# Performance work log

Hardware: AMD Instinct MI355X
Metric: run time of the kernel (lower is better)

Reference implementation:

```python
import jax, jax.numpy as jnp
import numpy as np
from jax import lax

FI, FO, K, EPS = 512, 256, 3, 1e-06


def _fir_kernel(gain):
    f = jnp.array([1.0, 3.0, 3.0, 1.0], dtype=jnp.float32)
    f = f[None, :] * f[:, None]
    f = f / f.sum() * gain  # (4,4), symmetric so conv-vs-correlation flip is a no-op
    return f


def setup_inputs() -> dict:
    key = jax.random.key(0)
    k1, k2 = jax.random.split(key)
    x = jax.random.normal(k1, (8, FI, 64, 64), dtype=jnp.float32)
    w = jax.random.normal(k2, (1, FO, FI, K, K), dtype=jnp.float32)
    return {"x": x, "w": w}


def reference(x, w):
    w_scale = (FI * K * K) ** (-0.5)
    wm = w[0] * w_scale  # (fo, fi, k, k); per-sample scale is constant across batch
    demod = lax.rsqrt(jnp.sum(wm * wm, axis=(1, 2, 3)) + EPS)  # (fo,)
    wm = wm * demod[:, None, None, None]
    # torch conv_transpose2d(stride=2, padding=0) with weight (fi, fo, k, k) where
    # weight[i, o] = wm[o, i]  ==  dilated conv with kernel flip(wm) OIHW, pad k-1=2.
    kern = wm[:, :, ::-1, ::-1]
    y = lax.conv_general_dilated(
        x, kern, window_strides=(1, 1), padding=[(2, 2), (2, 2)],
        lhs_dilation=(2, 2), dimension_numbers=("NCHW", "OIHW", "NCHW"))
    # upFirDn2D with scale=2, conv_k=3: p=0 -> pad (1,1) both dims, filter gain 4
    f = _fir_kernel(4.0)
    C = y.shape[1]
    fk = jnp.broadcast_to(f[None, None], (C, 1, 4, 4))
    y = lax.conv_general_dilated(
        y, fk, window_strides=(1, 1), padding=[(1, 1), (1, 1)],
        feature_group_count=C, dimension_numbers=("NCHW", "OIHW", "NCHW"))
    return y  # (8, 256, 128, 128)
```

## Files before the change

### kernel.cpp

```cpp
#include <hip/hip_runtime.h>

typedef unsigned short u16;
typedef unsigned int u32;
typedef __attribute__((ext_vector_type(8))) short bf16x8;
typedef __attribute__((ext_vector_type(4))) float f32x4;

#define XP_BYTES 35684352
#define YB_BYTES 68714544
#define HY_OFF   (XP_BYTES + YB_BYTES)
#define WS_NEED  ((size_t)HY_OFF + 2359296)
#define CS 16776

__device__ inline u16 f2bf(float f) {
  union { float f; unsigned u; } v; v.f = f;
  unsigned r = v.u + 0x7fffu + ((v.u >> 16) & 1u);
  return (u16)(r >> 16);
}

__device__ inline void gl_lds16(const u16* g, u16* l) {
  __builtin_amdgcn_global_load_lds(
      (const __attribute__((address_space(1))) unsigned int*)g,
      (__attribute__((address_space(3))) unsigned int*)l, 16, 0, 0);
}

__global__ void xprep(const float* __restrict__ x, u16* __restrict__ xp) {
  __shared__ float tile[64 * 65];
  int bid = blockIdx.x;
  int cc = bid & 7, h = (bid >> 3) & 63, n = bid >> 9;
  int c0 = cc * 64;
  int t = threadIdx.x;
  const float* xb = x + ((size_t)(n * 512 + c0) * 64 + h) * 64;
  for (int r = 0; r < 16; ++r) {
    int flat = r * 256 + t;
    int ci = flat >> 6, w = flat & 63;
    tile[w * 65 + ci] = xb[(size_t)ci * 4096 + w];
  }
  __syncthreads();
  u16* xpb = xp + ((size_t)(n * 66 + h + 1) * 66 + 1) * 512 + c0;
  for (int r = 0; r < 8; ++r) {
    int flat = r * 256 + t;
    int pr = flat & 31;
    int w = flat >> 5;
    int ci = pr * 2;
    float v0 = tile[w * 65 + ci], v1 = tile[w * 65 + ci + 1];
    unsigned pk = (unsigned)f2bf(v0) | ((unsigned)f2bf(v1) << 16);
    *(unsigned*)(xpb + (size_t)w * 512 + ci) = pk;
  }
  u16* rowbase = xp + ((size_t)(n * 66 + h + 1) * 66) * 512 + c0;
  if (t < 32) *(u32*)(rowbase + 2 * t) = 0u;
  else if (t < 64) *(u32*)(rowbase + (size_t)65 * 512 + 2 * (t - 32)) = 0u;
  if (h == 0) {
    u16* r0 = xp + ((size_t)(n * 66) * 66) * 512 + c0;
    for (int j = t; j < 2112; j += 256) {
      int col = j >> 5, wi = j & 31;
      *(u32*)(r0 + (size_t)col * 512 + 2 * wi) = 0u;
    }
  }
  if (h == 63) {
    u16* r65 = xp + ((size_t)(n * 66 + 65) * 66) * 512 + c0;
    for (int j = t; j < 2112; j += 256) {
      int col = j >> 5, wi = j & 31;
      *(u32*)(r65 + (size_t)col * 512 + 2 * wi) = 0u;
    }
  }
}

__global__ void wprep9(const float* __restrict__ w, u16* __restrict__ Hy) {
  __shared__ float wl[4608];
  __shared__ float red[256];
  int o = blockIdx.x, t = threadIdx.x;
  const float* wo = w + (size_t)o * 4608;
  float s = 0.f;
  for (int j = t; j < 4608; j += 256) { float v = wo[j]; wl[j] = v; s += v * v; }
  red[t] = s;
  __syncthreads();
  for (int st = 128; st; st >>= 1) { if (t < st) red[t] += red[t + st]; __syncthreads(); }
  float demod = rsqrtf(red[0] * (1.0f / 4608.0f) + 1e-6f);
  float scale = demod * 0.014731391274719739f;
  const int DY[9] = {0, 2, 0, 2, 0, 2, 1, 1, 1};
  const int DX[9] = {0, 0, 2, 2, 1, 1, 0, 2, 1};
  for (int i = t; i < 512; i += 256) {
#pragma unroll
    for (int pl = 0; pl < 9; ++pl) {
      float g = wl[i * 9 + DY[pl] * 3 + DX[pl]] * scale;
      Hy[(size_t)pl * 131072 + (size_t)o * 512 + i] = f2bf(g);
    }
  }
}

#define BARR() __builtin_amdgcn_s_barrier()
#define WAITL() do { asm volatile("s_waitcnt lgkmcnt(0)" ::: "memory"); __builtin_amdgcn_sched_barrier(0); } while (0)
#define WAITV4() do { asm volatile("s_waitcnt vmcnt(4)" ::: "memory"); __builtin_amdgcn_sched_barrier(0); } while (0)
#define WAITV0() do { asm volatile("s_waitcnt vmcnt(0)" ::: "memory"); __builtin_amdgcn_sched_barrier(0); } while (0)

__device__ __forceinline__ void rdA8(const u16* sb, int rbase, int grp, bf16x8 af[4][2]) {
#pragma unroll
  for (int ti = 0; ti < 4; ++ti) {
    int r = rbase + ti * 16;
    int x7 = r & 7;
#pragma unroll
    for (int ks = 0; ks < 2; ++ks) {
      int ch = (ks * 4 + grp) ^ x7;
      af[ti][ks] = *(const bf16x8*)(sb + r * 64 + ch * 8);
    }
  }
}

__device__ __forceinline__ void rdB4(const u16* sb, int rbase, int grp, bf16x8 bfr[2][2]) {
#pragma unroll
  for (int tj = 0; tj < 2; ++tj) {
    int r = rbase + tj * 16;
    int x7 = r & 7;
#pragma unroll
    for (int ks = 0; ks < 2; ++ks) {
      int ch = (ks * 4 + grp) ^ x7;
      bfr[tj][ks] = *(const bf16x8*)(sb + 16384 + r * 64 + ch * 8);
    }
  }
}

template <int MI, int NI>
__device__ __forceinline__ void qmfma(const bf16x8 af[4][2], const bf16x8 bfr[2][2],
                                      f32x4 acc[8][4]) {
#pragma unroll
  for (int ti = 0; ti < 4; ++ti)
#pragma unroll
    for (int tj = 0; tj < 2; ++tj)
#pragma unroll
      for (int ks = 0; ks < 2; ++ks)
        acc[MI * 4 + ti][NI * 2 + tj] = __builtin_amdgcn_mfma_f32_16x16x32_bf16(
            af[ti][ks], bfr[tj][ks], acc[MI * 4 + ti][NI * 2 + tj], 0, 0, 0);
}

__device__ __forceinline__ void stA2(const u16* __restrict__ xp, u16* d0, u16* d1,
                                     int tile, int NK, u32 a0, u32 a1,
                                     u32 adj1, u32 adj2, u32 adj3) {
  if (tile < NK) {
    int tap = tile >> 3;
    u32 ko = (u32)((tile & 7) << 6);
    u32 adj = tap == 0 ? 0u : (tap == 1 ? adj1 : (tap == 2 ? adj2 : adj3));
    gl_lds16(xp + (a0 - adj + ko), d0);
    gl_lds16(xp + (a1 - adj + ko), d1);
  }
}

__device__ __forceinline__ void stB2(const u16* __restrict__ hb, u16* d0, u16* d1,
                                     int tile, int NK, u32 b0, u32 b1) {
  if (tile < NK) {
    int tap = tile >> 3;
    u32 ko = (u32)((tile & 7) << 6);
    const u16* hp = hb + (size_t)tap * 131072;
    gl_lds16(hp + (b0 + ko), d0);
    gl_lds16(hp + (b1 + ko), d1);
  }
}

__global__ __launch_bounds__(512, 2) void conv_y(const u16* __restrict__ xp,
                                                 const u16* __restrict__ Hy,
                                                 u16* __restrict__ yb) {
  __shared__ __align__(16) u16 su[65536];

  int bid = blockIdx.x;
  int t = threadIdx.x;
  int wid = t >> 6, lane = t & 63;

  int img = bid & 7;
  int kk = bid >> 3;
  int mt, Wp, CNT, NTAP, PB, PO, STLIM;
  u32 adj1 = 0, adj2 = 0, adj3 = 0;
  if (kk < 17)      { mt = kk;      Wp = 66; CNT = 4290; NTAP = 4; PB = 0; PO = 0;     STLIM = 4296;
                      adj1 = 33792u; adj2 = 512u; adj3 = 34304u; }
  else if (kk < 34) { mt = kk - 17; Wp = 64; CNT = 4160; NTAP = 2; PB = 4; PO = 4296;  STLIM = 4160;
                      adj1 = 33792u; }
  else if (kk < 51) { mt = kk - 34; Wp = 66; CNT = 4224; NTAP = 2; PB = 6; PO = 8456;  STLIM = 4224;
                      adj1 = 512u; }
  else              { mt = kk - 51; Wp = 64; CNT = 4096; NTAP = 1; PB = 8; PO = 12680; STLIM = 4096; }

  int m0 = mt * 256;
  int NK = NTAP * 8;
  int NITER = NTAP * 4;
  const u16* hb = Hy + (size_t)PB * 131072;

  int wm = wid >> 2, wn = wid & 3;
  int la = lane & 15, grp = lane >> 4;

  int rho = t >> 3;
  int gch = (t & 7) ^ (rho & 7);

  u32 gA[4], gB[4];
#pragma unroll
  for (int i = 0; i < 4; ++i) {
    int m = m0 + i * 64 + rho;
    if (m > CNT - 1) m = CNT - 1;
    u32 a = (u32)m / (u32)Wp;
    u32 b = (u32)m - a * (u32)Wp;
    gA[i] = (u32)(((img * 66 + a + 1) * 66 + (b + 1)) * 512 + gch * 8);
    gB[i] = (u32)((i * 64 + rho) * 512 + gch * 8);
  }
  u16* sw = su + wid * 512;

  f32x4 acc[8][4];
#pragma unroll
  for (int i = 0; i < 8; ++i)
#pragma unroll
    for (int j = 0; j < 4; ++j) acc[i][j] = (f32x4){0.f, 0.f, 0.f, 0.f};

  stB2(hb, sw + 16384, sw + 20480, 0, NK, gB[0], gB[1]);
  stB2(hb, sw + 24576, sw + 28672, 0, NK, gB[2], gB[3]);
  stA2(xp, sw, sw + 4096, 0, NK, gA[0], gA[1], adj1, adj2, adj3);
  stA2(xp, sw + 8192, sw + 12288, 0, NK, gA[2], gA[3], adj1, adj2, adj3);
  stB2(hb, sw + 49152, sw + 53248, 1, NK, gB[0], gB[1]);
  stB2(hb, sw + 57344, sw + 61440, 1, NK, gB[2], gB[3]);
  WAITV4();
  BARR();

  bf16x8 af[4][2], bf0[2][2], bf1[2][2];

#pragma unroll 1
  for (int it = 0; it < NITER; ++it) {
    int t0 = 2 * it;
    bool more = (it + 1 < NITER);

    rdA8(su, wm * 128 + la, grp, af);
    rdB4(su, wn * 64 + la, grp, bf0);
    stA2(xp, sw + 32768, sw + 36864, t0 + 1, NK, gA[0], gA[1], adj1, adj2, adj3);
    BARR(); WAITL();
    __builtin_amdgcn_s_setprio(1); qmfma<0, 0>(af, bf0, acc); __builtin_amdgcn_s_setprio(0);
    BARR();
    rdB4(su, wn * 64 + 32 + la, grp, bf1);
    stA2(xp, sw + 40960, sw + 45056, t0 + 1, NK, gA[2], gA[3], adj1, adj2, adj3);
    BARR(); WAITL();
    __builtin_amdgcn_s_setprio(1); qmfma<0, 1>(af, bf1, acc); __builtin_amdgcn_s_setprio(0);
    BARR();
    rdA8(su, wm * 128 + 64 + la, grp, af);
    stB2(hb, sw + 16384, sw + 20480, t0 + 2, NK, gB[0], gB[1]);
    BARR(); WAITL();
    __builtin_amdgcn_s_setprio(1); qmfma<1, 1>(af, bf1, acc); __builtin_amdgcn_s_setprio(0);
    BARR();
    stB2(hb, sw + 24576, sw + 28672, t0 + 2, NK, gB[2], gB[3]);
    BARR(); WAITL();
    __builtin_amdgcn_s_setprio(1); qmfma<1, 0>(af, bf0, acc); __builtin_amdgcn_s_setprio(0);
    if (more) { WAITV4(); } else { WAITV0(); }
    BARR();
    rdA8(su + 32768, wm * 128 + la, grp, af);
    rdB4(su + 32768, wn * 64 + la, grp, bf0);
    stA2(xp, sw, sw + 4096, t0 + 2, NK, gA[0], gA[1], adj1, adj2, adj3);
    BARR(); WAITL();
    __builtin_amdgcn_s_setprio(1); qmfma<0, 0>(af, bf0, acc); __builtin_amdgcn_s_setprio(0);
    BARR();
    rdB4(su + 32768, wn * 64 + 32 + la, grp, bf1);
    stA2(xp, sw + 8192, sw + 12288, t0 + 2, NK, gA[2], gA[3], adj1, adj2, adj3);
    BARR(); WAITL();
    __builtin_amdgcn_s_setprio(1); qmfma<0, 1>(af, bf1, acc); __builtin_amdgcn_s_setprio(0);
    BARR();
    rdA8(su + 32768, wm * 128 + 64 + la, grp, af);
    stB2(hb, sw + 49152, sw + 53248, t0 + 3, NK, gB[0], gB[1]);
    BARR(); WAITL();
    __builtin_amdgcn_s_setprio(1); qmfma<1, 1>(af, bf1, acc); __builtin_amdgcn_s_setprio(0);
    BARR();
    stB2(hb, sw + 57344, sw + 61440, t0 + 3, NK, gB[2], gB[3]);
    BARR(); WAITL();
    __builtin_amdgcn_s_setprio(1); qmfma<1, 0>(af, bf0, acc); __builtin_amdgcn_s_setprio(0);
    if (more) { WAITV4(); }
    BARR();
  }

  WAITV0();
  __syncthreads();
#pragma unroll
  for (int nj = 0; nj < 4; ++nj) {
    int orow = wn * 64 + nj * 16 + la;
    int x7 = orow & 7;
#pragma unroll
    for (int mi8 = 0; mi8 < 8; ++mi8)
#pragma unroll
      for (int jp = 0; jp < 2; ++jp) {
        int ml = wm * 128 + mi8 * 16 + grp * 4 + jp * 2;
        u32 pk = (u32)f2bf(acc[mi8][nj][jp * 2]) |
                 ((u32)f2bf(acc[mi8][nj][jp * 2 + 1]) << 16);
        *(u32*)(su + orow * 256 + (((ml >> 3) ^ x7) * 8) + (ml & 7)) = pk;
      }
  }
  __syncthreads();
  {
    u16* ybp = yb + 8;
    int o = t >> 1, s = t & 1;
    size_t gb = (size_t)(img * 256 + o) * CS + PO + m0 + s * 128;
    int x7 = o & 7;
#pragma unroll
    for (int i = 0; i < 16; ++i) {
      int mo = s * 128 + i * 8;
      if (m0 + mo < STLIM)
        *(bf16x8*)(ybp + gb + i * 8) = *(const bf16x8*)(su + o * 256 + (((mo >> 3) ^ x7) * 8));
    }
  }
}

__global__ void fir2(const u16* __restrict__ yb, float* __restrict__ z) {
  int flat = blockIdx.x * 256 + threadIdx.x;
  int qh = flat & 15, phb = (flat >> 4) & 31, o = (flat >> 9) & 255, n = flat >> 17;
  const u16* cb = yb + 8 + (size_t)(n * 256 + o) * CS;
  int a0 = 2 * phb - 1;
  int b0 = 4 * qh - 1;

  float out[4][8];
#pragma unroll
  for (int i = 0; i < 4; ++i)
#pragma unroll
    for (int j = 0; j < 8; ++j) out[i][j] = 0.f;

  const int PO_[4] = {0, 4296, 8456, 12680};
  const int WP_[4] = {66, 64, 66, 64};
  const int HA_[4] = {65, 65, 64, 64};
  const int WB_[4] = {65, 64, 65, 64};

#pragma unroll
  for (int ph = 0; ph < 4; ++ph) {
    int rp = ph >> 1, rq = ph & 1;
    const u16* pb = cb + PO_[ph];
    float hcol[4][8];
#pragma unroll
    for (int la = 0; la < 4; ++la) {
      if (rp == 0 && la == 0) continue;
      int ag = a0 + la;
      bool rv = (ag >= 0) && (ag < HA_[ph]);
      const u16* rb = pb + (ag * WP_[ph] + b0 - 1);
      u32 ls[4];
      ls[0] = *(const u32*)(rb);
      ls[1] = *(const u32*)(rb + 2);
      ls[2] = *(const u32*)(rb + 4);
      ls[3] = *(const u32*)(rb + 6);
      float v[6];
#pragma unroll
      for (int lb = 0; lb < 6; ++lb) {
        int jj = lb + 1;
        u32 w16 = (jj & 1) ? (ls[jj >> 1] >> 16) : (ls[jj >> 1] & 0xffffu);
        float fv = __uint_as_float(w16 << 16);
        int bg = b0 + lb;
        bool ok = rv && (bg >= 0) && (bg < WB_[ph]);
        v[lb] = ok ? fv : 0.f;
      }
#pragma unroll
      for (int e = 0; e < 4; ++e) {
        if (rq == 0) {
          hcol[la][2 * e]     = 3.f * v[e + 1] + v[e + 2];
          hcol[la][2 * e + 1] = v[e + 1] + 3.f * v[e + 2];
        } else {
          hcol[la][2 * e]     = v[e] + 3.f * v[e + 1];
          hcol[la][2 * e + 1] = 3.f * v[e + 1] + v[e + 2];
        }
      }
    }
#pragma unroll
    for (int jq = 0; jq < 8; ++jq) {
      if (rp == 0) {
        out[0][jq] += 3.f * hcol[1][jq] + hcol[2][jq];
        out[1][jq] += hcol[1][jq] + 3.f * hcol[2][jq];
        out[2][jq] += 3.f * hcol[2][jq] + hcol[3][jq];
        out[3][jq] += hcol[2][jq] + 3.f * hcol[3][jq];
      } else {
        out[0][jq] += hcol[0][jq] + 3.f * hcol[1][jq];
        out[1][jq] += 3.f * hcol[1][jq] + hcol[2][jq];
        out[2][jq] += hcol[1][jq] + 3.f * hcol[2][jq];
        out[3][jq] += 3.f * hcol[2][jq] + hcol[3][jq];
      }
    }
  }

  float* zb = z + ((size_t)(n * 256 + o) * 128 + phb * 4) * 128 + qh * 8;
#pragma unroll
  for (int ip = 0; ip < 4; ++ip) {
    f32x4 v0, v1;
#pragma unroll
    for (int j = 0; j < 4; ++j) { v0[j] = out[ip][j] * 0.0625f; v1[j] = out[ip][j + 4] * 0.0625f; }
    *(f32x4*)(zb + (size_t)ip * 128) = v0;
    *(f32x4*)(zb + (size_t)ip * 128 + 4) = v1;
  }
}

__global__ void wprep36(const float* __restrict__ w, u16* __restrict__ Hm) {
  __shared__ float wl[4608];
  __shared__ float red[256];
  int o = blockIdx.x, t = threadIdx.x;
  const float* wo = w + (size_t)o * 4608;
  float s = 0.f;
  for (int j = t; j < 4608; j += 256) { float v = wo[j]; wl[j] = v; s += v * v; }
  red[t] = s;
  __syncthreads();
  for (int st = 128; st; st >>= 1) { if (t < st) red[t] += red[t + st]; __syncthreads(); }
  float demod = rsqrtf(red[0] * (1.0f / 4608.0f) + 1e-6f);
  float scale = demod * 0.014731391274719739f;
  const float F1[4] = {1.f, 3.f, 3.f, 1.f};
  for (int i = t; i < 512; i += 256) {
    float wm[9];
    for (int k = 0; k < 9; ++k) wm[k] = wl[i * 9 + k] * scale;
    for (int rp = 0; rp < 2; ++rp)
      for (int rq = 0; rq < 2; ++rq)
        for (int u = 0; u < 3; ++u)
          for (int v = 0; v < 3; ++v) {
            int s_ = 2 - 2 * u + rp, t_ = 2 - 2 * v + rq;
            float g = 0.f;
            for (int dy = 0; dy < 3; ++dy) {
              int a = dy + 1 - s_;
              if (a < 0 || a > 3) continue;
              for (int dx = 0; dx < 3; ++dx) {
                int b = dx + 1 - t_;
                if (b < 0 || b > 3) continue;
                g += wm[dy * 3 + dx] * (F1[a] * F1[b]);
              }
            }
            g *= 0.0625f;
            Hm[(size_t)((rp * 2 + rq) * 9 + u * 3 + v) * 131072 + (size_t)o * 512 + i] = f2bf(g);
          }
  }
}

__global__ __launch_bounds__(256) void conv_main(const u16* __restrict__ xp,
                                                 const u16* __restrict__ Hm,
                                                 float* __restrict__ z) {
  __shared__ __align__(16) float smemf[8448];
  u16* su = (u16*)smemf;
  int bid = blockIdx.x;
  int sub = bid & 7;
  int rp = sub >> 2;
  int o0 = (sub & 3) * 64;
  int mtile = bid >> 3;
  int n_img = mtile >> 5;
  int hp0 = (mtile & 31) * 2;
  int t = threadIdx.x;
  int wave = t >> 6, lane = t & 63;
  int wm0 = (wave & 1) * 64;
  int wn0 = (wave >> 1) * 32;
  int la = lane & 15;
  int ks = (lane >> 4) * 8;
  int rsel = t >> 2;
  int koff = (t & 3) * 8;
  f32x4 acc[2][4][2];
#pragma unroll
  for (int a = 0; a < 2; ++a)
#pragma unroll
    for (int b = 0; b < 4; ++b)
#pragma unroll
      for (int c = 0; c < 2; ++c)
        acc[a][b][c] = (f32x4){0.f, 0.f, 0.f, 0.f};
#pragma unroll 1
  for (int tap = 0; tap < 9; ++tap) {
    int du = tap / 3, dv = tap - du * 3;
    const u16* gA0 = xp + ((size_t)(n_img * 66 + hp0 + du) * 66 + dv) * 512;
    const u16* gB0 = Hm + (size_t)(rp * 18 + tap) * 131072 + (size_t)(o0 + rsel) * 512 + koff;
    const u16* gAr0 = gA0 + (size_t)rsel * 512 + koff;
    const u16* gAr1 = gA0 + (size_t)(66 + rsel) * 512 + koff;
#pragma unroll 1
    for (int kc = 0; kc < 16; ++kc) {
      int c0 = kc * 32;
      __syncthreads();
      gl_lds16(gAr0 + c0, su + wave * 512);
      gl_lds16(gAr1 + c0, su + 2048 + wave * 512);
      gl_lds16(gB0 + c0,              su + 4096 + wave * 512);
      gl_lds16(gB0 + 9 * 131072 + c0, su + 6144 + wave * 512);
      __syncthreads();
      bf16x8 af[4];
#pragma unroll
      for (int ti = 0; ti < 4; ++ti)
        af[ti] = *(const bf16x8*)(su + (wm0 + ti * 16 + la) * 32 + ks);
      bf16x8 bfr[2][2];
#pragma unroll
      for (int rqq = 0; rqq < 2; ++rqq)
#pragma unroll
        for (int tj = 0; tj < 2; ++tj)
          bfr[rqq][tj] = *(const bf16x8*)(su + 4096 + rqq * 2048 + (wn0 + tj * 16 + la) * 32 + ks);
#pragma unroll
      for (int rqq = 0; rqq < 2; ++rqq)
#pragma unroll
        for (int ti = 0; ti < 4; ++ti)
#pragma unroll
          for (int tj = 0; tj < 2; ++tj)
            acc[rqq][ti][tj] = __builtin_amdgcn_mfma_f32_16x16x32_bf16(
                af[ti], bfr[rqq][tj], acc[rqq][ti][tj], 0, 0, 0);
    }
  }
  __syncthreads();
  float* lws = smemf + wave * 2112;
  int p = 2 * (hp0 + (wave & 1)) + rp;
#pragma unroll
  for (int tj = 0; tj < 2; ++tj) {
#pragma unroll
    for (int rqq = 0; rqq < 2; ++rqq)
#pragma unroll
      for (int ti = 0; ti < 4; ++ti) {
        int wqb = ti * 16 + (lane >> 4) * 4;
        f32x4 v = acc[rqq][ti][tj];
#pragma unroll
        for (int r = 0; r < 4; ++r)
          lws[la * 132 + 2 * (wqb + r) + rqq] = v[r];
      }
    __syncthreads();
    int obase = o0 + wn0 + tj * 16;
#pragma unroll
    for (int c = 0; c < 8; ++c) {
      int idx = c * 64 + lane;
      int ol = idx >> 5, q4 = (idx & 31) * 4;
      f32x4 vv = *(const f32x4*)(lws + ol * 132 + q4);
      *(f32x4*)(z + (((size_t)n_img * 256 + obase + ol) * 128 + p) * 128 + q4) = vv;
    }
    __syncthreads();
  }
}

extern "C" void kernel_launch(void* const* d_in, const int* in_sizes, int n_in,
                              void* d_out, int out_size, void* d_ws, size_t ws_size,
                              hipStream_t stream) {
  const float* x = (const float*)d_in[0];
  const float* w = (const float*)d_in[1];
  float* z = (float*)d_out;
  u16* xp = (u16*)d_ws;

  if (ws_size >= WS_NEED) {
    u16* yb = (u16*)((char*)d_ws + XP_BYTES);
    u16* hy = (u16*)((char*)d_ws + HY_OFF);
    xprep<<<4096, 256, 0, stream>>>(x, xp);
    wprep9<<<256, 256, 0, stream>>>(w, hy);
    conv_y<<<536, 512, 0, stream>>>(xp, hy, yb);
    fir2<<<4096, 256, 0, stream>>>(yb, z);
  } else {
    u16* Hm = (u16*)((char*)d_ws + XP_BYTES);
    hipMemsetAsync(xp, 0, XP_BYTES, stream);
    xprep<<<4096, 256, 0, stream>>>(x, xp);
    wprep36<<<256, 256, 0, stream>>>(w, Hm);
    conv_main<<<2048, 256, 0, stream>>>(xp, Hm, z);
  }
}
```

Measured before the change: 315.0 us.

## Halve conv GEMM N-tile and K-step to fit more blocks per CU

The conv_y GEMM tile shrinks from 256x256 to 256x128 output channels and the K step from 64 to 32. Shared memory drops from 128KB to 48KB and launch bounds rise to 4 blocks per SM, doubling the grid to 1072 blocks. The aim is higher occupancy and better CU fill, with more blocks to hide memory latency. The cost is halved reuse of A tiles, twice as many pipeline iterations with barriers, and an epilogue split into two passes.

```diff
diff --git a/kernel.cpp b/kernel.cpp
--- a/kernel.cpp
+++ b/kernel.cpp
@@ -90,75 +90,56 @@
 
 #define BARR() __builtin_amdgcn_s_barrier()
 #define WAITL() do { asm volatile("s_waitcnt lgkmcnt(0)" ::: "memory"); __builtin_amdgcn_sched_barrier(0); } while (0)
-#define WAITV4() do { asm volatile("s_waitcnt vmcnt(4)" ::: "memory"); __builtin_amdgcn_sched_barrier(0); } while (0)
+#define WAITV1() do { asm volatile("s_waitcnt vmcnt(1)" ::: "memory"); __builtin_amdgcn_sched_barrier(0); } while (0)
 #define WAITV0() do { asm volatile("s_waitcnt vmcnt(0)" ::: "memory"); __builtin_amdgcn_sched_barrier(0); } while (0)
 
-__device__ __forceinline__ void rdA8(const u16* sb, int rbase, int grp, bf16x8 af[4][2]) {
+__device__ __forceinline__ void rdA4(const u16* sb, int rbase, int grp, bf16x8 af[4]) {
 #pragma unroll
   for (int ti = 0; ti < 4; ++ti) {
     int r = rbase + ti * 16;
-    int x7 = r & 7;
-#pragma unroll
-    for (int ks = 0; ks < 2; ++ks) {
-      int ch = (ks * 4 + grp) ^ x7;
-      af[ti][ks] = *(const bf16x8*)(sb + r * 64 + ch * 8);
-    }
-  }
-}
-
-__device__ __forceinline__ void rdB4(const u16* sb, int rbase, int grp, bf16x8 bfr[2][2]) {
-#pragma unroll
-  for (int tj = 0; tj < 2; ++tj) {
-    int r = rbase + tj * 16;
-    int x7 = r & 7;
-#pragma unroll
-    for (int ks = 0; ks < 2; ++ks) {
-      int ch = (ks * 4 + grp) ^ x7;
-      bfr[tj][ks] = *(const bf16x8*)(sb + 16384 + r * 64 + ch * 8);
-    }
-  }
+    int ch = grp ^ (r & 3);
+    af[ti] = *(const bf16x8*)(sb + r * 32 + ch * 8);
+  }
+}
+
+__device__ __forceinline__ bf16x8 rdB1(const u16* sb, int r, int grp) {
+  int ch = grp ^ (r & 3);
+  return *(const bf16x8*)(sb + 8192 + r * 32 + ch * 8);
 }
 
 template <int MI, int NI>
-__device__ __forceinline__ void qmfma(const bf16x8 af[4][2], const bf16x8 bfr[2][2],
-                                      f32x4 acc[8][4]) {
+__device__ __forceinline__ void qmfma4(const bf16x8 af[4], bf16x8 bf,
+                                       f32x4 acc[8][2]) {
 #pragma unroll
   for (int ti = 0; ti < 4; ++ti)
-#pragma unroll
-    for (int tj = 0; tj < 2; ++tj)
-#pragma unroll
-      for (int ks = 0; ks < 2; ++ks)
-        acc[MI * 4 + ti][NI * 2 + tj] = __builtin_amdgcn_mfma_f32_16x16x32_bf16(
-            af[ti][ks], bfr[tj][ks], acc[MI * 4 + ti][NI * 2 + tj], 0, 0, 0);
-}
-
-__device__ __forceinline__ void stA2(const u16* __restrict__ xp, u16* d0, u16* d1,
-                                     int tile, int NK, u32 a0, u32 a1,
+    acc[MI * 4 + ti][NI] = __builtin_amdgcn_mfma_f32_16x16x32_bf16(
+        af[ti], bf, acc[MI * 4 + ti][NI], 0, 0, 0);
+}
+
+__device__ __forceinline__ void stA1(const u16* __restrict__ xp, u16* d,
+                                     int tile, int NK, u32 a,
                                      u32 adj1, u32 adj2, u32 adj3) {
   if (tile < NK) {
-    int tap = tile >> 3;
-    u32 ko = (u32)((tile & 7) << 6);
+    int tap = tile >> 4;
+    u32 ko = (u32)((tile & 15) << 5);
     u32 adj = tap == 0 ? 0u : (tap == 1 ? adj1 : (tap == 2 ? adj2 : adj3));
-    gl_lds16(xp + (a0 - adj + ko), d0);
-    gl_lds16(xp + (a1 - adj + ko), d1);
-  }
-}
-
-__device__ __forceinline__ void stB2(const u16* __restrict__ hb, u16* d0, u16* d1,
-                                     int tile, int NK, u32 b0, u32 b1) {
+    gl_lds16(xp + (a - adj + ko), d);
+  }
+}
+
+__device__ __forceinline__ void stB1(const u16* __restrict__ hb, u16* d,
+                                     int tile, int NK, u32 b) {
   if (tile < NK) {
-    int tap = tile >> 3;
-    u32 ko = (u32)((tile & 7) << 6);
-    const u16* hp = hb + (size_t)tap * 131072;
-    gl_lds16(hp + (b0 + ko), d0);
-    gl_lds16(hp + (b1 + ko), d1);
-  }
-}
-
-__global__ __launch_bounds__(512, 2) void conv_y(const u16* __restrict__ xp,
+    int tap = tile >> 4;
+    u32 ko = (u32)((tile & 15) << 5);
+    gl_lds16(hb + (size_t)tap * 131072 + (b + ko), d);
+  }
+}
+
+__global__ __launch_bounds__(512, 4) void conv_y(const u16* __restrict__ xp,
                                                  const u16* __restrict__ Hy,
                                                  u16* __restrict__ yb) {
-  __shared__ __align__(16) u16 su[65536];
+  __shared__ __align__(16) u16 su[24576];
 
   int bid = blockIdx.x;
   int t = threadIdx.x;
@@ -166,133 +147,141 @@
 
   int img = bid & 7;
   int kk = bid >> 3;
-  int mt, Wp, CNT, NTAP, PB, PO, STLIM;
+  int mt, oh, Wp, CNT, NTAP, PB, PO, STLIM;
   u32 adj1 = 0, adj2 = 0, adj3 = 0;
-  if (kk < 17)      { mt = kk;      Wp = 66; CNT = 4290; NTAP = 4; PB = 0; PO = 0;     STLIM = 4296;
-                      adj1 = 33792u; adj2 = 512u; adj3 = 34304u; }
-  else if (kk < 34) { mt = kk - 17; Wp = 64; CNT = 4160; NTAP = 2; PB = 4; PO = 4296;  STLIM = 4160;
-                      adj1 = 33792u; }
-  else if (kk < 51) { mt = kk - 34; Wp = 66; CNT = 4224; NTAP = 2; PB = 6; PO = 8456;  STLIM = 4224;
-                      adj1 = 512u; }
-  else              { mt = kk - 51; Wp = 64; CNT = 4096; NTAP = 1; PB = 8; PO = 12680; STLIM = 4096; }
+  if (kk < 34)       { int k2 = kk;       mt = k2 >> 1; oh = k2 & 1; Wp = 66; CNT = 4290; NTAP = 4; PB = 0; PO = 0;     STLIM = 4296;
+                       adj1 = 33792u; adj2 = 512u; adj3 = 34304u; }
+  else if (kk < 68)  { int k2 = kk - 34;  mt = k2 >> 1; oh = k2 & 1; Wp = 64; CNT = 4160; NTAP = 2; PB = 4; PO = 4296;  STLIM = 4160;
+                       adj1 = 33792u; }
+  else if (kk < 102) { int k2 = kk - 68;  mt = k2 >> 1; oh = k2 & 1; Wp = 66; CNT = 4224; NTAP = 2; PB = 6; PO = 8456;  STLIM = 4224;
+                       adj1 = 512u; }
+  else               { int k2 = kk - 102; mt = k2 >> 1; oh = k2 & 1; Wp = 64; CNT = 4096; NTAP = 1; PB = 8; PO = 12680; STLIM = 4096; }
 
   int m0 = mt * 256;
-  int NK = NTAP * 8;
-  int NITER = NTAP * 4;
+  int o0 = oh * 128;
+  int NK = NTAP * 16;
+  int NITER = NTAP * 8;
   const u16* hb = Hy + (size_t)PB * 131072;
 
   int wm = wid >> 2, wn = wid & 3;
   int la = lane & 15, grp = lane >> 4;
 
-  int rho = t >> 3;
-  int gch = (t & 7) ^ (rho & 7);
-
-  u32 gA[4], gB[4];
-#pragma unroll
-  for (int i = 0; i < 4; ++i) {
-    int m = m0 + i * 64 + rho;
+  int rho = t >> 2;
+  int gch = (t & 3) ^ (rho & 3);
+
+  u32 gA0, gA1, gB;
+  {
+    int m = m0 + rho;
     if (m > CNT - 1) m = CNT - 1;
     u32 a = (u32)m / (u32)Wp;
     u32 b = (u32)m - a * (u32)Wp;
-    gA[i] = (u32)(((img * 66 + a + 1) * 66 + (b + 1)) * 512 + gch * 8);
-    gB[i] = (u32)((i * 64 + rho) * 512 + gch * 8);
-  }
-  u16* sw = su + wid * 512;
-
-  f32x4 acc[8][4];
+    gA0 = (u32)(((img * 66 + a + 1) * 66 + (b + 1)) * 512 + gch * 8);
+    m = m0 + 128 + rho;
+    if (m > CNT - 1) m = CNT - 1;
+    a = (u32)m / (u32)Wp;
+    b = (u32)m - a * (u32)Wp;
+    gA1 = (u32)(((img * 66 + a + 1) * 66 + (b + 1)) * 512 + gch * 8);
+    gB = (u32)((o0 + rho) * 512 + gch * 8);
+  }
+  int ws = wid * 512;
+
+  f32x4 acc[8][2];
 #pragma unroll
   for (int i = 0; i < 8; ++i)
 #pragma unroll
-    for (int j = 0; j < 4; ++j) acc[i][j] = (f32x4){0.f, 0.f, 0.f, 0.f};
-
-  stB2(hb, sw + 16384, sw + 20480, 0, NK, gB[0], gB[1]);
-  stB2(hb, sw + 24576, sw + 28672, 0, NK, gB[2], gB[3]);
-  stA2(xp, sw, sw + 4096, 0, NK, gA[0], gA[1], adj1, adj2, adj3);
-  stA2(xp, sw + 8192, sw + 12288, 0, NK, gA[2], gA[3], adj1, adj2, adj3);
-  stB2(hb, sw + 49152, sw + 53248, 1, NK, gB[0], gB[1]);
-  stB2(hb, sw + 57344, sw + 61440, 1, NK, gB[2], gB[3]);
-  WAITV4();
+    for (int j = 0; j < 2; ++j) acc[i][j] = (f32x4){0.f, 0.f, 0.f, 0.f};
+
+  stB1(hb, su + 8192 + ws, 0, NK, gB);
+  stA1(xp, su + 0 + ws, 0, NK, gA0, adj1, adj2, adj3);
+  stA1(xp, su + 4096 + ws, 0, NK, gA1, adj1, adj2, adj3);
+  stB1(hb, su + 20480 + ws, 1, NK, gB);
+  WAITV1();
   BARR();
 
-  bf16x8 af[4][2], bf0[2][2], bf1[2][2];
+  bf16x8 af[4], bf0, bf1;
 
 #pragma unroll 1
   for (int it = 0; it < NITER; ++it) {
     int t0 = 2 * it;
     bool more = (it + 1 < NITER);
 
-    rdA8(su, wm * 128 + la, grp, af);
-    rdB4(su, wn * 64 + la, grp, bf0);
-    stA2(xp, sw + 32768, sw + 36864, t0 + 1, NK, gA[0], gA[1], adj1, adj2, adj3);
+    rdA4(su, wm * 128 + la, grp, af);
+    bf0 = rdB1(su, wn * 32 + la, grp);
+    stA1(xp, su + 12288 + ws, t0 + 1, NK, gA0, adj1, adj2, adj3);
     BARR(); WAITL();
-    __builtin_amdgcn_s_setprio(1); qmfma<0, 0>(af, bf0, acc); __builtin_amdgcn_s_setprio(0);
+    __builtin_amdgcn_s_setprio(1); qmfma4<0, 0>(af, bf0, acc); __builtin_amdgcn_s_setprio(0);
     BARR();
-    rdB4(su, wn * 64 + 32 + la, grp, bf1);
-    stA2(xp, sw + 40960, sw + 45056, t0 + 1, NK, gA[2], gA[3], adj1, adj2, adj3);
+    bf1 = rdB1(su, wn * 32 + 16 + la, grp);
+    stA1(xp, su + 16384 + ws, t0 + 1, NK, gA1, adj1, adj2, adj3);
     BARR(); WAITL();
-    __builtin_amdgcn_s_setprio(1); qmfma<0, 1>(af, bf1, acc); __builtin_amdgcn_s_setprio(0);
+    __builtin_amdgcn_s_setprio(1); qmfma4<0, 1>(af, bf1, acc); __builtin_amdgcn_s_setprio(0);
     BARR();
-    rdA8(su, wm * 128 + 64 + la, grp, af);
-    stB2(hb, sw + 16384, sw + 20480, t0 + 2, NK, gB[0], gB[1]);
+    rdA4(su, wm * 128 + 64 + la, grp, af);
+    stB1(hb, su + 8192 + ws, t0 + 2, NK, gB);
     BARR(); WAITL();
-    __builtin_amdgcn_s_setprio(1); qmfma<1, 1>(af, bf1, acc); __builtin_amdgcn_s_setprio(0);
+    __builtin_amdgcn_s_setprio(1);
+    qmfma4<1, 1>(af, bf1, acc); qmfma4<1, 0>(af, bf0, acc);
+    __builtin_amdgcn_s_setprio(0);
+    if (more) { WAITV1(); } else { WAITV0(); }
     BARR();
-    stB2(hb, sw + 24576, sw + 28672, t0 + 2, NK, gB[2], gB[3]);
+    rdA4(su + 12288, wm * 128 + la, grp, af);
+    bf0 = rdB1(su + 12288, wn * 32 + la, grp);
+    stA1(xp, su + 0 + ws, t0 + 2, NK, gA0, adj1, adj2, adj3);
     BARR(); WAITL();
-    __builtin_amdgcn_s_setprio(1); qmfma<1, 0>(af, bf0, acc); __builtin_amdgcn_s_setprio(0);
-    if (more) { WAITV4(); } else { WAITV0(); }
+    __builtin_amdgcn_s_setprio(1); qmfma4<0, 0>(af, bf0, acc); __builtin_amdgcn_s_setprio(0);
     BARR();
-    rdA8(su + 32768, wm * 128 + la, grp, af);
-    rdB4(su + 32768, wn * 64 + la, grp, bf0);
-    stA2(xp, sw, sw + 4096, t0 + 2, NK, gA[0], gA[1], adj1, adj2, adj3);
+    bf1 = rdB1(su + 12288, wn * 32 + 16 + la, grp);
+    stA1(xp, su + 4096 + ws, t0 + 2, NK, gA1, adj1, adj2, adj3);
     BARR(); WAITL();
-    __builtin_amdgcn_s_setprio(1); qmfma<0, 0>(af, bf0, acc); __builtin_amdgcn_s_setprio(0);
+    __builtin_amdgcn_s_setprio(1); qmfma4<0, 1>(af, bf1, acc); __builtin_amdgcn_s_setprio(0);
     BARR();
-    rdB4(su + 32768, wn * 64 + 32 + la, grp, bf1);
-    stA2(xp, sw + 8192, sw + 12288, t0 + 2, NK, gA[2], gA[3], adj1, adj2, adj3);
+    rdA4(su + 12288, wm * 128 + 64 + la, grp, af);
+    stB1(hb, su + 20480 + ws, t0 + 3, NK, gB);
     BARR(); WAITL();
-    __builtin_amdgcn_s_setprio(1); qmfma<0, 1>(af, bf1, acc); __builtin_amdgcn_s_setprio(0);
-    BARR();
-    rdA8(su + 32768, wm * 128 + 64 + la, grp, af);
-    stB2(hb, sw + 49152, sw + 53248, t0 + 3, NK, gB[0], gB[1]);
-    BARR(); WAITL();
-    __builtin_amdgcn_s_setprio(1); qmfma<1, 1>(af, bf1, acc); __builtin_amdgcn_s_setprio(0);
-    BARR();
-    stB2(hb, sw + 57344, sw + 61440, t0 + 3, NK, gB[2], gB[3]);
-    BARR(); WAITL();
-    __builtin_amdgcn_s_setprio(1); qmfma<1, 0>(af, bf0, acc); __builtin_amdgcn_s_setprio(0);
-    if (more) { WAITV4(); }
+    __builtin_amdgcn_s_setprio(1);
+    qmfma4<1, 1>(af, bf1, acc); qmfma4<1, 0>(af, bf0, acc);
+    __builtin_amdgcn_s_setprio(0);
+    if (more) { WAITV1(); }
     BARR();
   }
 
   WAITV0();
   __syncthreads();
-#pragma unroll
-  for (int nj = 0; nj < 4; ++nj) {
-    int orow = wn * 64 + nj * 16 + la;
-    int x7 = orow & 7;
-#pragma unroll
-    for (int mi8 = 0; mi8 < 8; ++mi8)
-#pragma unroll
-      for (int jp = 0; jp < 2; ++jp) {
-        int ml = wm * 128 + mi8 * 16 + grp * 4 + jp * 2;
-        u32 pk = (u32)f2bf(acc[mi8][nj][jp * 2]) |
-                 ((u32)f2bf(acc[mi8][nj][jp * 2 + 1]) << 16);
-        *(u32*)(su + orow * 256 + (((ml >> 3) ^ x7) * 8) + (ml & 7)) = pk;
+  u16* ybp = yb + 8;
+#pragma unroll 1
+  for (int r = 0; r < 2; ++r) {
+    if ((wn >> 1) == r) {
+      int base_orl = (wn & 1) * 32;
+#pragma unroll
+      for (int nj = 0; nj < 2; ++nj) {
+        int orl = base_orl + nj * 16 + la;
+        int x7 = orl & 7;
+#pragma unroll
+        for (int mi8 = 0; mi8 < 8; ++mi8)
+#pragma unroll
+          for (int jp = 0; jp < 2; ++jp) {
+            int ml = wm * 128 + mi8 * 16 + grp * 4 + jp * 2;
+            u32 pk = (u32)f2bf(acc[mi8][nj][jp * 2]) |
+                     ((u32)f2bf(acc[mi8][nj][jp * 2 + 1]) << 16);
+            *(u32*)(su + orl * 256 + (((ml >> 3) ^ x7) * 8) + (ml & 7)) = pk;
+          }
       }
-  }
-  __syncthreads();
-  {
-    u16* ybp = yb + 8;
-    int o = t >> 1, s = t & 1;
-    size_t gb = (size_t)(img * 256 + o) * CS + PO + m0 + s * 128;
-    int x7 = o & 7;
-#pragma unroll
-    for (int i = 0; i < 16; ++i) {
-      int mo = s * 128 + i * 8;
-      if (m0 + mo < STLIM)
-        *(bf16x8*)(ybp + gb + i * 8) = *(const bf16x8*)(su + o * 256 + (((mo >> 3) ^ x7) * 8));
-    }
+    }
+    __syncthreads();
+    {
+      int ol = t >> 3, s2 = t & 7;
+      int og = o0 + r * 64 + ol;
+      size_t gb = (size_t)(img * 256 + og) * CS + PO + m0;
+      int x7 = ol & 7;
+#pragma unroll
+      for (int i = 0; i < 4; ++i) {
+        int cidx = s2 * 4 + i;
+        int m = cidx * 8;
+        if (m0 + m < STLIM)
+          *(bf16x8*)(ybp + gb + m) = *(const bf16x8*)(su + ol * 256 + ((cidx ^ x7) * 8));
+      }
+    }
+    if (r == 0) __syncthreads();
   }
 }
 
@@ -520,7 +509,7 @@
     u16* hy = (u16*)((char*)d_ws + HY_OFF);
     xprep<<<4096, 256, 0, stream>>>(x, xp);
     wprep9<<<256, 256, 0, stream>>>(w, hy);
-    conv_y<<<536, 512, 0, stream>>>(xp, hy, yb);
+    conv_y<<<1072, 512, 0, stream>>>(xp, hy, yb);
     fir2<<<4096, 256, 0, stream>>>(yb, z);
   } else {
     u16* Hm = (u16*)((char*)d_ws + XP_BYTES);
```

New measurement: 324.9 us. 1.03x slower.
